# Optimization experiments

Measured on AMD Instinct MI355X. Metric: run time of the kernel, lower is better.

Reference implementation:

```python
import jax, jax.numpy as jnp
import numpy as np

COST_COORDINATE = 1.0  # init kwarg cost_coordinate


def _lsa(cost):
    """Rectangular linear sum assignment (Jonker-Volgenant shortest augmenting
    path), matching scipy.optimize.linear_sum_assignment's algorithm/output.
    Returns (row_ind, col_ind) sorted by row_ind, length = min(nr, nc)."""
    cost = np.asarray(cost, dtype=np.float64)
    transposed = cost.shape[0] > cost.shape[1]
    if transposed:
        cost = cost.T
    nr, nc = cost.shape
    u = np.zeros(nr)
    v = np.zeros(nc)
    path = np.full(nc, -1, dtype=np.int64)
    col4row = np.full(nr, -1, dtype=np.int64)
    row4col = np.full(nc, -1, dtype=np.int64)
    for cur_row in range(nr):
        shortest = np.full(nc, np.inf)
        SR = np.zeros(nr, dtype=bool)
        SC = np.zeros(nc, dtype=bool)
        remaining = np.ones(nc, dtype=bool)
        min_val = 0.0
        i = cur_row
        sink = -1
        while sink == -1:
            SR[i] = True
            rem = np.nonzero(remaining)[0]
            cand = min_val + cost[i, rem] - u[i] - v[rem]
            better = cand < shortest[rem]
            idx_b = rem[better]
            shortest[idx_b] = cand[better]
            path[idx_b] = i
            j = rem[np.argmin(shortest[rem])]
            min_val = shortest[j]
            if not np.isfinite(min_val):
                raise RuntimeError('cost matrix is infeasible')
            SC[j] = True
            remaining[j] = False
            if row4col[j] == -1:
                sink = j
            else:
                i = row4col[j]
        # dual updates
        u[cur_row] += min_val
        mask = SR.copy()
        mask[cur_row] = False
        u[mask] += min_val - shortest[col4row[mask]]
        v[SC] -= min_val - shortest[SC]
        # augment along alternating path
        j = sink
        while True:
            i = path[j]
            row4col[j] = i
            col4row[i], j = j, col4row[i]
            if i == cur_row:
                break
    if transposed:
        order = np.argsort(col4row)
        return col4row[order], order.astype(np.int64)
    return np.arange(nr, dtype=np.int64), col4row


def setup_inputs() -> dict:
    key = jax.random.key(0)
    k1, k2 = jax.random.split(key)
    outputs = jax.random.uniform(k1, (16, 4096, 4), dtype=jnp.float32)  # [B, Q, 4]
    targets = jax.random.uniform(k2, (16, 128, 4), dtype=jnp.float32)   # [B, nt, 4]
    return {'outputs': outputs, 'targets': targets}


@jax.jit
def _cost_matrix(outputs, targets):
    # Block-diagonal part of torch.cdist(out.flatten(0,1), cat(targets), p=1):
    # only the per-image [Q, nt] blocks survive the .split(sizes, -1) in the
    # original, so we compute exactly those. C[b,q,t] = sum_d |out - tgt|.
    return COST_COORDINATE * jnp.abs(
        outputs[:, :, None, :] - targets[:, None, :, :]
    ).sum(-1)  # [B, Q, nt]


def reference(outputs, targets):
    C = _cost_matrix(outputs, targets)
    Cn = np.asarray(jax.device_get(C), dtype=np.float64)
    rows, cols = [], []
    for b in range(Cn.shape[0]):  # batch loop mirrors the original scipy loop
        r, c = _lsa(Cn[b])
        rows.append(r)
        cols.append(c)
    row_ind = jnp.asarray(np.stack(rows), dtype=jnp.int64)  # [B, min(Q,nt)]
    col_ind = jnp.asarray(np.stack(cols), dtype=jnp.int64)  # [B, min(Q,nt)]
    return C, row_ind, col_ind
```

## Files before the change

### kernel.cpp

```cpp
#include <hip/hip_runtime.h>
#include <math.h>

#define NB   16
#define NQ   4096
#define NTGT 128
#define CELEMS (NB * NQ * NTGT)

#define NSLOT 64
#define AT   512
#define ACPT 8
#define ANW  (AT / 64)
#define NCOST (CELEMS / 4 / 2048)

typedef unsigned long long u64;

__global__ __launch_bounds__(256) void rowmin_kernel(
    const float* __restrict__ outputs,
    const float* __restrict__ targets,
    u64*   __restrict__ rowkey2)
{
    __shared__ u64 part[4][NTGT];
    const int tid  = threadIdx.x;
    const int t4   = tid & 31;
    const int b    = blockIdx.x >> 6;
    const int blk  = blockIdx.x & (NSLOT - 1);
    const int idx0 = blockIdx.x * 2048 + tid;

    const float4* tg = reinterpret_cast<const float4*>(targets) + (b << 7) + (t4 << 2);
    float4 g[4];
    #pragma unroll
    for (int f = 0; f < 4; ++f) g[f] = tg[f];

    u64 keymin[4] = {~0ull, ~0ull, ~0ull, ~0ull};

    #pragma unroll
    for (int e = 0; e < 8; ++e) {
        int idx = idx0 + 256 * e;
        int bq  = idx >> 5;
        float4 o = reinterpret_cast<const float4*>(outputs)[bq];
        u64 q = (u64)(unsigned)(bq & (NQ - 1));
        #pragma unroll
        for (int f = 0; f < 4; ++f) {
            float4 gg = g[f];
            float r = (fabsf(o.x - gg.x) + fabsf(o.y - gg.y)) +
                      (fabsf(o.z - gg.z) + fabsf(o.w - gg.w));
            u64 key = (((u64)__float_as_uint(r)) << 32) | q;
            if (key < keymin[f]) keymin[f] = key;
        }
    }

    #pragma unroll
    for (int f = 0; f < 4; ++f) {
        u64 ov = __shfl_xor(keymin[f], 32);
        if (ov < keymin[f]) keymin[f] = ov;
    }
    if ((tid & 63) < 32) {
        int w = tid >> 6;
        #pragma unroll
        for (int f = 0; f < 4; ++f) part[w][(t4 << 2) + f] = keymin[f];
    }
    __syncthreads();

    if (tid < NTGT) {
        u64 k = part[0][tid];
        #pragma unroll
        for (int s = 1; s < 4; ++s) { u64 ov = part[s][tid]; if (ov < k) k = ov; }
        rowkey2[(((size_t)b * NSLOT) + blk) * NTGT + tid] = k;
    }
}

__global__ __launch_bounds__(AT, 1) void fused_kernel(
    const float* __restrict__ outputs,
    const float* __restrict__ targets,
    const u64*   __restrict__ rowkey2,
    float* __restrict__ C,
    float* __restrict__ row_out,
    float* __restrict__ col_out)
{
    __shared__ unsigned claim_[NQ];
    __shared__ short  row4col_[NQ];
    __shared__ unsigned char path_[NQ];
    __shared__ unsigned char vtouch_[NQ];
    __shared__ float4 tgt_[NTGT];
    __shared__ double u_[NTGT];
    __shared__ u64    red2_[4][NTGT];
    __shared__ int    rowarg_[NTGT];
    __shared__ short  col4row_[NTGT];
    __shared__ short  left_[NTGT];
    __shared__ int    sc_j[NTGT];
    __shared__ double sc_v[NTGT];
    __shared__ u64    redk_[2][ANW];
    __shared__ u64    bmask_[2];

    const int tid = threadIdx.x;

    if (blockIdx.x >= NB) {
        const int blk = blockIdx.x - NB;
        const int t4  = tid & 31;
        const float4* tg = reinterpret_cast<const float4*>(targets);
        float4 g0, g1, g2, g3;
        {
            int b = (blk * 2048 + tid) >> 17;
            const float4* tgb = tg + (b << 7) + (t4 << 2);
            g0 = tgb[0]; g1 = tgb[1]; g2 = tgb[2]; g3 = tgb[3];
        }
        #pragma unroll
        for (int e = 0; e < 4; ++e) {
            int f  = blk * 2048 + e * 512 + tid;
            int bq = f >> 5;
            float4 o = reinterpret_cast<const float4*>(outputs)[bq];
            float4 r;
            r.x = (fabsf(o.x - g0.x) + fabsf(o.y - g0.y)) + (fabsf(o.z - g0.z) + fabsf(o.w - g0.w));
            r.y = (fabsf(o.x - g1.x) + fabsf(o.y - g1.y)) + (fabsf(o.z - g1.z) + fabsf(o.w - g1.w));
            r.z = (fabsf(o.x - g2.x) + fabsf(o.y - g2.y)) + (fabsf(o.z - g2.z) + fabsf(o.w - g2.w));
            r.w = (fabsf(o.x - g3.x) + fabsf(o.y - g3.y)) + (fabsf(o.z - g3.z) + fabsf(o.w - g3.w));
            reinterpret_cast<float4*>(C)[f] = r;
        }
        return;
    }

    const int b = blockIdx.x;
    const float4* outq = reinterpret_cast<const float4*>(outputs) + b * NQ;

    float4 o0 = outq[tid];
    float4 o1 = outq[tid + AT];
    float4 o2 = outq[tid + AT * 2];
    float4 o3 = outq[tid + AT * 3];
    float4 o4 = outq[tid + AT * 4];
    float4 o5 = outq[tid + AT * 5];
    float4 o6 = outq[tid + AT * 6];
    float4 o7 = outq[tid + AT * 7];
    double sh0 = 0, sh1 = 0, sh2 = 0, sh3 = 0, sh4 = 0, sh5 = 0, sh6 = 0, sh7 = 0;
    double vv0 = 0, vv1 = 0, vv2 = 0, vv3 = 0, vv4 = 0, vv5 = 0, vv6 = 0, vv7 = 0;

    #pragma unroll
    for (int kk = 0; kk < ACPT; ++kk) {
        int k = tid + AT * kk;
        row4col_[k] = -1;
        claim_[k] = 0xFFFFFFFFu;
        vtouch_[k] = 0;
    }

    {
        const int t = tid & 127, s = tid >> 7;
        const u64* rk = rowkey2 + (size_t)b * NSLOT * NTGT;
        u64 k = ~0ull;
        #pragma unroll
        for (int gg = 0; gg < NSLOT / 4; ++gg) {
            u64 ov = rk[(s * (NSLOT / 4) + gg) * NTGT + t];
            if (ov < k) k = ov;
        }
        red2_[s][t] = k;
    }
    __syncthreads();

    if (tid < NTGT) {
        u64 key = red2_[0][tid];
        #pragma unroll
        for (int s = 1; s < 4; ++s) { u64 ov = red2_[s][tid]; if (ov < key) key = ov; }
        u_[tid] = (double)__uint_as_float((unsigned)(key >> 32));
        rowarg_[tid] = (int)(key & 0xffffffffu);
        tgt_[tid] = reinterpret_cast<const float4*>(targets)[b * NTGT + tid];
    }
    __syncthreads();

    if (tid < NTGT) atomicMin(&claim_[rowarg_[tid]], (unsigned)tid);
    __syncthreads();

    bool un = false;
    if (tid < NTGT) {
        int j = rowarg_[tid];
        bool won = (claim_[j] == (unsigned)tid);
        col4row_[tid] = won ? (short)j : (short)-1;
        if (won) row4col_[j] = (short)tid;
        un = !won;
    }
    {
        u64 m = __ballot(un);
        if ((tid & 63) == 0 && (tid >> 6) < 2) bmask_[tid >> 6] = m;
    }
    __syncthreads();
    const int nleft = __popcll(bmask_[0]) + __popcll(bmask_[1]);
    if (un) {
        int lane = tid & 63, w = tid >> 6;
        int r = __popcll(bmask_[w] & ((1ull << lane) - 1)) + (w ? __popcll(bmask_[0]) : 0);
        left_[r] = (short)tid;
    }
    __syncthreads();

    int parity = 0;

#define COSTN(g, on) ((fabsf((on).x - (g).x) + fabsf((on).y - (g).y)) + \
                      (fabsf((on).z - (g).z) + fabsf((on).w - (g).w)))

    for (int li = 0; li < nleft; ++li) {
        const int cur = left_[li];
        const int j0  = rowarg_[cur];
        const bool fast = (vtouch_[j0] == 0);
        int      i;
        double   minv = 0.0;
        int      fj   = -1;
        int      Lns  = 0;
        unsigned rem  = 0xFFu;
        unsigned pend = 0u;
        bool     first = true;

        const double uc = u_[cur];
        const float4 gc = tgt_[cur];

        if (fast) {
            i = row4col_[j0];
            fj = j0; Lns = 1;
            const bool mine = ((j0 & (AT - 1)) == tid);
            const int  slot = j0 >> 9;
            if (mine) {
                rem  &= ~(1u << slot);
                pend |=  (1u << slot);
                path_[j0] = (unsigned char)cur;
                #define SETJ0(n, shn) if (slot == n) shn = 0.0;
                SETJ0(0, sh0) SETJ0(1, sh1) SETJ0(2, sh2) SETJ0(3, sh3)
                SETJ0(4, sh4) SETJ0(5, sh5) SETJ0(6, sh6) SETJ0(7, sh7)
                #undef SETJ0
            }
            if (tid == 0) { sc_j[0] = j0; sc_v[0] = 0.0; }
        } else {
            i = cur;
        }

        while (true) {
            const double ui = u_[i];
            const float4 g  = tgt_[i];

            double bv = (double)INFINITY;
            int    bi = 0xFFF;

            if (first && fast) {
                #define FSTEP(n, on, shn, vvn)                                  \
                {   int k = tid + AT * n;                                       \
                    double cand_c = ((0.0 + (double)COSTN(gc, on)) - uc) - vvn; \
                    double cand_w = ((0.0 + (double)COSTN(g,  on)) - ui) - vvn; \
                    bool wless = cand_w < cand_c;                               \
                    double s = wless ? cand_w : cand_c;                         \
                    if ((rem >> n) & 1u) {                                      \
                        shn = s;                                                \
                        path_[k] = (unsigned char)(wless ? i : cur);            \
                        if (s < bv) { bv = s; bi = k; }                         \
                    }                                                           \
                }
                FSTEP(0, o0, sh0, vv0) FSTEP(1, o1, sh1, vv1)
                FSTEP(2, o2, sh2, vv2) FSTEP(3, o3, sh3, vv3)
                FSTEP(4, o4, sh4, vv4) FSTEP(5, o5, sh5, vv5)
                FSTEP(6, o6, sh6, vv6) FSTEP(7, o7, sh7, vv7)
                #undef FSTEP
            } else if (first) {
                #define ISTEP(n, on, shn, vvn)                                  \
                {   int k = tid + AT * n;                                       \
                    double s = ((0.0 + (double)COSTN(gc, on)) - uc) - vvn;      \
                    shn = s;                                                    \
                    path_[k] = (unsigned char)cur;                              \
                    if (s < bv) { bv = s; bi = k; }                             \
                }
                ISTEP(0, o0, sh0, vv0) ISTEP(1, o1, sh1, vv1)
                ISTEP(2, o2, sh2, vv2) ISTEP(3, o3, sh3, vv3)
                ISTEP(4, o4, sh4, vv4) ISTEP(5, o5, sh5, vv5)
                ISTEP(6, o6, sh6, vv6) ISTEP(7, o7, sh7, vv7)
                #undef ISTEP
            } else {
                #define USTEP(n, on, shn, vvn)                                  \
                {   int k = tid + AT * n;                                       \
                    double cand = ((minv + (double)COSTN(g, on)) - ui) - vvn;   \
                    bool valid = (rem >> n) & 1u;                               \
                    if (valid && cand < shn) {                                  \
                        shn = cand;                                             \
                        path_[k] = (unsigned char)i;                            \
                    }                                                           \
                    if (valid && shn < bv) { bv = shn; bi = k; }                \
                }
                USTEP(0, o0, sh0, vv0) USTEP(1, o1, sh1, vv1)
                USTEP(2, o2, sh2, vv2) USTEP(3, o3, sh3, vv3)
                USTEP(4, o4, sh4, vv4) USTEP(5, o5, sh5, vv5)
                USTEP(6, o6, sh6, vv6) USTEP(7, o7, sh7, vv7)
                #undef USTEP
            }
            first = false;

            u64 key = (__double_as_longlong(bv) & ~0xFFFull) | (unsigned)bi;
            #pragma unroll
            for (int off = 32; off > 0; off >>= 1) {
                u64 ok = __shfl_down(key, off);
                if (ok < key) key = ok;
            }
            if ((tid & 63) == 0) redk_[parity][tid >> 6] = key;
            __syncthreads();

            u64 fkey = redk_[parity][0];
            #pragma unroll
            for (int w = 1; w < ANW; ++w) {
                u64 ok = redk_[parity][w];
                if (ok < fkey) fkey = ok;
            }
            parity ^= 1;

            fj   = (int)(fkey & 0xFFFull);
            minv = __longlong_as_double((long long)(fkey & ~0xFFFull));

            int r = row4col_[fj];
            if ((fj & (AT - 1)) == tid) {
                rem &= ~(1u << (fj >> 9));
                if (r >= 0) pend |= (1u << (fj >> 9));
            }
            if (r < 0) break;
            if (tid == 0) { sc_j[Lns] = fj; sc_v[Lns] = minv; }
            Lns++;
            i = r;
        }

        const double dfin = minv;
        #define VPAT(n, shn, vvn)                                               \
        if (pend & (1u << n)) {                                                 \
            vvn -= dfin - shn;                                                  \
            vtouch_[tid + AT * n] = 1;                                          \
        }
        VPAT(0, sh0, vv0) VPAT(1, sh1, vv1) VPAT(2, sh2, vv2) VPAT(3, sh3, vv3)
        VPAT(4, sh4, vv4) VPAT(5, sh5, vv5) VPAT(6, sh6, vv6) VPAT(7, sh7, vv7)
        #undef VPAT
        if (tid == 0) {
            u_[cur] += dfin;
            for (int e = 0; e < Lns; ++e) {
                int j = sc_j[e];
                u_[row4col_[j]] += dfin - sc_v[e];
            }
            int j = fj;
            while (true) {
                int i2 = path_[j];
                row4col_[j] = (short)i2;
                int nj = col4row_[i2];
                col4row_[i2] = (short)j;
                j = nj;
                if (i2 == cur) break;
            }
        }
        __syncthreads();
    }
#undef COSTN

    if (tid < NTGT) {
        int val = col4row_[tid];
        int rank = 0;
        #pragma unroll
        for (int k = 0; k < NTGT; ++k) rank += (col4row_[k] < val);
        row_out[b * NTGT + rank] = (float)val;
        col_out[b * NTGT + rank] = (float)tid;
    }
}

extern "C" void kernel_launch(void* const* d_in, const int* in_sizes, int n_in,
                              void* d_out, int out_size, void* d_ws, size_t ws_size,
                              hipStream_t stream) {
    const float* outputs = (const float*)d_in[0];
    const float* targets = (const float*)d_in[1];
    float* out = (float*)d_out;

    u64* rowkey2 = (u64*)d_ws;

    hipLaunchKernelGGL(rowmin_kernel, dim3(NB * NSLOT), dim3(256), 0, stream,
                       outputs, targets, rowkey2);
    hipLaunchKernelGGL(fused_kernel, dim3(NB + NCOST), dim3(AT), 0, stream,
                       outputs, targets, rowkey2, out,
                       out + CELEMS, out + CELEMS + NB * NTGT);
}
```

Before: 31.04 us.

## Halve LSA block width, pack row4col into reduction key, use atomicMin triple-buffer

Measured after the change: 43.19 us. 39.1% more time.

```diff
diff --git a/kernel.cpp b/kernel.cpp
--- a/kernel.cpp
+++ b/kernel.cpp
@@ -7,10 +7,9 @@
 #define CELEMS (NB * NQ * NTGT)
 
 #define NSLOT 64
-#define AT   512
-#define ACPT 8
-#define ANW  (AT / 64)
-#define NCOST (CELEMS / 4 / 2048)
+#define AT   256
+#define ACPT 16
+#define NCOST 1024
 
 typedef unsigned long long u64;
 
@@ -83,13 +82,13 @@
     __shared__ unsigned char vtouch_[NQ];
     __shared__ float4 tgt_[NTGT];
     __shared__ double u_[NTGT];
-    __shared__ u64    red2_[4][NTGT];
+    __shared__ u64    red2_[2][NTGT];
     __shared__ int    rowarg_[NTGT];
     __shared__ short  col4row_[NTGT];
     __shared__ short  left_[NTGT];
-    __shared__ int    sc_j[NTGT];
+    __shared__ short  sc_i[NTGT];
     __shared__ double sc_v[NTGT];
-    __shared__ u64    redk_[2][ANW];
+    __shared__ u64    redk_[3];
     __shared__ u64    bmask_[2];
 
     const int tid = threadIdx.x;
@@ -105,8 +104,8 @@
             g0 = tgb[0]; g1 = tgb[1]; g2 = tgb[2]; g3 = tgb[3];
         }
         #pragma unroll
-        for (int e = 0; e < 4; ++e) {
-            int f  = blk * 2048 + e * 512 + tid;
+        for (int e = 0; e < 8; ++e) {
+            int f  = blk * 2048 + e * 256 + tid;
             int bq = f >> 5;
             float4 o = reinterpret_cast<const float4*>(outputs)[bq];
             float4 r;
@@ -122,16 +121,16 @@
     const int b = blockIdx.x;
     const float4* outq = reinterpret_cast<const float4*>(outputs) + b * NQ;
 
-    float4 o0 = outq[tid];
-    float4 o1 = outq[tid + AT];
-    float4 o2 = outq[tid + AT * 2];
-    float4 o3 = outq[tid + AT * 3];
-    float4 o4 = outq[tid + AT * 4];
-    float4 o5 = outq[tid + AT * 5];
-    float4 o6 = outq[tid + AT * 6];
-    float4 o7 = outq[tid + AT * 7];
-    double sh0 = 0, sh1 = 0, sh2 = 0, sh3 = 0, sh4 = 0, sh5 = 0, sh6 = 0, sh7 = 0;
-    double vv0 = 0, vv1 = 0, vv2 = 0, vv3 = 0, vv4 = 0, vv5 = 0, vv6 = 0, vv7 = 0;
+#define FORALL(M) \
+    M(0,oo0,sh0,vv0,rc0)   M(1,oo1,sh1,vv1,rc1)   M(2,oo2,sh2,vv2,rc2)   M(3,oo3,sh3,vv3,rc3) \
+    M(4,oo4,sh4,vv4,rc4)   M(5,oo5,sh5,vv5,rc5)   M(6,oo6,sh6,vv6,rc6)   M(7,oo7,sh7,vv7,rc7) \
+    M(8,oo8,sh8,vv8,rc8)   M(9,oo9,sh9,vv9,rc9)   M(10,oo10,sh10,vv10,rc10) M(11,oo11,sh11,vv11,rc11) \
+    M(12,oo12,sh12,vv12,rc12) M(13,oo13,sh13,vv13,rc13) M(14,oo14,sh14,vv14,rc14) M(15,oo15,sh15,vv15,rc15)
+
+#define DECL(n, on, shn, vvn, rcn) \
+    float4 on = outq[tid + AT * n]; double shn = 0.0, vvn = 0.0; int rcn = -1;
+    FORALL(DECL)
+#undef DECL
 
     #pragma unroll
     for (int kk = 0; kk < ACPT; ++kk) {
@@ -140,14 +139,15 @@
         claim_[k] = 0xFFFFFFFFu;
         vtouch_[k] = 0;
     }
+    if (tid == 0) { redk_[0] = ~0ull; redk_[1] = ~0ull; redk_[2] = ~0ull; }
 
     {
         const int t = tid & 127, s = tid >> 7;
         const u64* rk = rowkey2 + (size_t)b * NSLOT * NTGT;
         u64 k = ~0ull;
         #pragma unroll
-        for (int gg = 0; gg < NSLOT / 4; ++gg) {
-            u64 ov = rk[(s * (NSLOT / 4) + gg) * NTGT + t];
+        for (int gg = 0; gg < NSLOT / 2; ++gg) {
+            u64 ov = rk[(s * (NSLOT / 2) + gg) * NTGT + t];
             if (ov < k) k = ov;
         }
         red2_[s][t] = k;
@@ -156,8 +156,7 @@
 
     if (tid < NTGT) {
         u64 key = red2_[0][tid];
-        #pragma unroll
-        for (int s = 1; s < 4; ++s) { u64 ov = red2_[s][tid]; if (ov < key) key = ov; }
+        u64 ov  = red2_[1][tid]; if (ov < key) key = ov;
         u_[tid] = (double)__uint_as_float((unsigned)(key >> 32));
         rowarg_[tid] = (int)(key & 0xffffffffu);
         tgt_[tid] = reinterpret_cast<const float4*>(targets)[b * NTGT + tid];
@@ -188,7 +187,10 @@
     }
     __syncthreads();
 
-    int parity = 0;
+#define RELOAD(n, on, shn, vvn, rcn) rcn = row4col_[tid + AT * n];
+    FORALL(RELOAD)
+
+    unsigned s3 = 0;
 
 #define COSTN(g, on) ((fabsf((on).x - (g).x) + fabsf((on).y - (g).y)) + \
                       (fabsf((on).z - (g).z) + fabsf((on).w - (g).w)))
@@ -201,7 +203,7 @@
         double   minv = 0.0;
         int      fj   = -1;
         int      Lns  = 0;
-        unsigned rem  = 0xFFu;
+        unsigned rem  = 0xFFFFu;
         unsigned pend = 0u;
         bool     first = true;
 
@@ -212,124 +214,110 @@
             i = row4col_[j0];
             fj = j0; Lns = 1;
             const bool mine = ((j0 & (AT - 1)) == tid);
-            const int  slot = j0 >> 9;
+            const int  slot = j0 >> 8;
             if (mine) {
                 rem  &= ~(1u << slot);
                 pend |=  (1u << slot);
                 path_[j0] = (unsigned char)cur;
-                #define SETJ0(n, shn) if (slot == n) shn = 0.0;
-                SETJ0(0, sh0) SETJ0(1, sh1) SETJ0(2, sh2) SETJ0(3, sh3)
-                SETJ0(4, sh4) SETJ0(5, sh5) SETJ0(6, sh6) SETJ0(7, sh7)
+                #define SETJ0(n, on, shn, vvn, rcn) if (slot == n) shn = 0.0;
+                FORALL(SETJ0)
                 #undef SETJ0
             }
-            if (tid == 0) { sc_j[0] = j0; sc_v[0] = 0.0; }
+            if (tid == 0) { sc_i[0] = (short)i; sc_v[0] = 0.0; }
         } else {
             i = cur;
         }
 
         while (true) {
+            if (tid == 0) redk_[s3 == 2 ? 0 : s3 + 1] = ~0ull;
             const double ui = u_[i];
             const float4 g  = tgt_[i];
 
             double bv = (double)INFINITY;
-            int    bi = 0xFFF;
+            int    bn = 0;
 
             if (first && fast) {
-                #define FSTEP(n, on, shn, vvn)                                  \
-                {   int k = tid + AT * n;                                       \
-                    double cand_c = ((0.0 + (double)COSTN(gc, on)) - uc) - vvn; \
+                #define FSTEP(n, on, shn, vvn, rcn)                             \
+                {   double cand_c = ((0.0 + (double)COSTN(gc, on)) - uc) - vvn; \
                     double cand_w = ((0.0 + (double)COSTN(g,  on)) - ui) - vvn; \
                     bool wless = cand_w < cand_c;                               \
                     double s = wless ? cand_w : cand_c;                         \
                     if ((rem >> n) & 1u) {                                      \
                         shn = s;                                                \
-                        path_[k] = (unsigned char)(wless ? i : cur);            \
-                        if (s < bv) { bv = s; bi = k; }                         \
+                        path_[tid + AT * n] = (unsigned char)(wless ? i : cur); \
+                        if (s < bv) { bv = s; bn = n; }                         \
                     }                                                           \
                 }
-                FSTEP(0, o0, sh0, vv0) FSTEP(1, o1, sh1, vv1)
-                FSTEP(2, o2, sh2, vv2) FSTEP(3, o3, sh3, vv3)
-                FSTEP(4, o4, sh4, vv4) FSTEP(5, o5, sh5, vv5)
-                FSTEP(6, o6, sh6, vv6) FSTEP(7, o7, sh7, vv7)
+                FORALL(FSTEP)
                 #undef FSTEP
             } else if (first) {
-                #define ISTEP(n, on, shn, vvn)                                  \
-                {   int k = tid + AT * n;                                       \
-                    double s = ((0.0 + (double)COSTN(gc, on)) - uc) - vvn;      \
+                #define ISTEP(n, on, shn, vvn, rcn)                             \
+                {   double s = ((0.0 + (double)COSTN(gc, on)) - uc) - vvn;      \
                     shn = s;                                                    \
-                    path_[k] = (unsigned char)cur;                              \
-                    if (s < bv) { bv = s; bi = k; }                             \
+                    path_[tid + AT * n] = (unsigned char)cur;                   \
+                    if (s < bv) { bv = s; bn = n; }                             \
                 }
-                ISTEP(0, o0, sh0, vv0) ISTEP(1, o1, sh1, vv1)
-                ISTEP(2, o2, sh2, vv2) ISTEP(3, o3, sh3, vv3)
-                ISTEP(4, o4, sh4, vv4) ISTEP(5, o5, sh5, vv5)
-                ISTEP(6, o6, sh6, vv6) ISTEP(7, o7, sh7, vv7)
+                FORALL(ISTEP)
                 #undef ISTEP
             } else {
-                #define USTEP(n, on, shn, vvn)                                  \
-                {   int k = tid + AT * n;                                       \
-                    double cand = ((minv + (double)COSTN(g, on)) - ui) - vvn;   \
+                #define USTEP(n, on, shn, vvn, rcn)                             \
+                {   double cand = ((minv + (double)COSTN(g, on)) - ui) - vvn;   \
                     bool valid = (rem >> n) & 1u;                               \
                     if (valid && cand < shn) {                                  \
                         shn = cand;                                             \
-                        path_[k] = (unsigned char)i;                            \
+                        path_[tid + AT * n] = (unsigned char)i;                 \
                     }                                                           \
-                    if (valid && shn < bv) { bv = shn; bi = k; }                \
+                    if (valid && shn < bv) { bv = shn; bn = n; }                \
                 }
-                USTEP(0, o0, sh0, vv0) USTEP(1, o1, sh1, vv1)
-                USTEP(2, o2, sh2, vv2) USTEP(3, o3, sh3, vv3)
-                USTEP(4, o4, sh4, vv4) USTEP(5, o5, sh5, vv5)
-                USTEP(6, o6, sh6, vv6) USTEP(7, o7, sh7, vv7)
+                FORALL(USTEP)
                 #undef USTEP
             }
             first = false;
 
-            u64 key = (__double_as_longlong(bv) & ~0xFFFull) | (unsigned)bi;
+            int bi = tid + (bn << 8);
+            int brc = -1;
+            #define SELR(n, on, shn, vvn, rcn) if (bn == n) brc = rcn;
+            FORALL(SELR)
+            #undef SELR
+            u64 key = (__double_as_longlong(bv) & ~0xFFFFFull)
+                    | ((u64)(unsigned)(brc + 1) << 12) | (unsigned)bi;
             #pragma unroll
             for (int off = 32; off > 0; off >>= 1) {
                 u64 ok = __shfl_down(key, off);
                 if (ok < key) key = ok;
             }
-            if ((tid & 63) == 0) redk_[parity][tid >> 6] = key;
+            if ((tid & 63) == 0) atomicMin(&redk_[s3], key);
             __syncthreads();
 
-            u64 fkey = redk_[parity][0];
-            #pragma unroll
-            for (int w = 1; w < ANW; ++w) {
-                u64 ok = redk_[parity][w];
-                if (ok < fkey) fkey = ok;
-            }
-            parity ^= 1;
+            u64 fkey = redk_[s3];
+            s3 = (s3 == 2) ? 0 : s3 + 1;
 
             fj   = (int)(fkey & 0xFFFull);
-            minv = __longlong_as_double((long long)(fkey & ~0xFFFull));
-
-            int r = row4col_[fj];
+            int r = (int)((fkey >> 12) & 0xFFull) - 1;
+            minv = __longlong_as_double((long long)(fkey & ~0xFFFFFull));
+
             if ((fj & (AT - 1)) == tid) {
-                rem &= ~(1u << (fj >> 9));
-                if (r >= 0) pend |= (1u << (fj >> 9));
+                rem &= ~(1u << (fj >> 8));
+                if (r >= 0) pend |= (1u << (fj >> 8));
             }
             if (r < 0) break;
-            if (tid == 0) { sc_j[Lns] = fj; sc_v[Lns] = minv; }
+            if (tid == 0) { sc_i[Lns] = (short)r; sc_v[Lns] = minv; }
             Lns++;
             i = r;
         }
 
         const double dfin = minv;
-        #define VPAT(n, shn, vvn)                                               \
+        #define VPAT(n, on, shn, vvn, rcn)                                      \
         if (pend & (1u << n)) {                                                 \
             vvn -= dfin - shn;                                                  \
             vtouch_[tid + AT * n] = 1;                                          \
         }
-        VPAT(0, sh0, vv0) VPAT(1, sh1, vv1) VPAT(2, sh2, vv2) VPAT(3, sh3, vv3)
-        VPAT(4, sh4, vv4) VPAT(5, sh5, vv5) VPAT(6, sh6, vv6) VPAT(7, sh7, vv7)
+        FORALL(VPAT)
         #undef VPAT
         if (tid == 0) {
             u_[cur] += dfin;
-            for (int e = 0; e < Lns; ++e) {
-                int j = sc_j[e];
-                u_[row4col_[j]] += dfin - sc_v[e];
-            }
+            for (int e = 0; e < Lns; ++e)
+                u_[sc_i[e]] += dfin - sc_v[e];
             int j = fj;
             while (true) {
                 int i2 = path_[j];
@@ -341,8 +329,11 @@
             }
         }
         __syncthreads();
-    }
+        FORALL(RELOAD)
+    }
+#undef RELOAD
 #undef COSTN
+#undef FORALL
 
     if (tid < NTGT) {
         int val = col4row_[tid];
```
